# Kernel optimization log

Hardware: AMD Instinct MI355X
Metric: run time of the kernel (lower is better)

Reference implementation:

```python
import jax, jax.numpy as jnp
import numpy as np

B, SQ, SD, H = 64, 64, 512, 128


def setup_inputs() -> dict:
    key = jax.random.key(0)
    k1, k2, k3, k4, k5 = jax.random.split(key, 5)
    q = jax.random.normal(k1, (B, SQ, H), dtype=jnp.float32)
    d_pos = jax.random.normal(k2, (B, SD, H), dtype=jnp.float32)
    d_neg = jax.random.normal(k3, (B, SD, H), dtype=jnp.float32)
    mask_pos = jax.random.randint(k4, (B, SD), 0, 2, dtype=jnp.int32).at[:, 0].set(1)
    mask_neg = jax.random.randint(k5, (B, SD), 0, 2, dtype=jnp.int32).at[:, 0].set(1)
    return {"q": q, "d_pos": d_pos, "d_neg": d_neg,
            "mask_pos": mask_pos, "mask_neg": mask_neg}


def _colbert_maxsim(q, d, mask):
    # q: [a, s, h], d: [b, t, h], mask: [b, t] -> scores [a, b]
    simis = jnp.einsum('ash,bth->abst', q, d)            # [a, b, s, t]
    simis = jnp.where(mask[None, :, None, :] == 0, -jnp.inf, simis)
    return simis.max(axis=3).sum(axis=2)                 # max over t, sum over s


def reference(q, d_pos, d_neg, mask_pos, mask_neg):
    # Concatenate pos and in-batch-negative score blocks -> [B, 2B]
    distances = jnp.concatenate(
        [_colbert_maxsim(q, d_pos, mask_pos),
         _colbert_maxsim(q, d_neg, mask_neg)], axis=1)
    labels = jnp.arange(q.shape[0])
    logp = jax.nn.log_softmax(distances, axis=1)
    loss = -jnp.take_along_axis(logp, labels[:, None], axis=1).mean()
    return loss
```

## Files before the change

kernel.cpp:

```cpp
#include <hip/hip_runtime.h>
#include <hip/hip_bf16.h>
#include <math.h>
#include <stdint.h>

#define BB 64
#define SQN 64
#define SDN 512
#define HH 128

typedef __attribute__((ext_vector_type(8))) short bf16x8;
typedef __attribute__((ext_vector_type(16))) float f32x16;

__device__ __forceinline__ short f2bf(float f) {
  union { float f; unsigned u; } x; x.f = f;
  unsigned r = x.u + 0x7fffu + ((x.u >> 16) & 1u);
  return (short)(r >> 16);
}

__device__ __forceinline__ void gl_lds16(const short* g, short* l) {
  __builtin_amdgcn_global_load_lds(
      (const __attribute__((address_space(1))) unsigned int*)g,
      (__attribute__((address_space(3))) unsigned int*)l, 16, 0, 0);
}

__global__ __launch_bounds__(256)
void convert_all(const float* __restrict__ q, const float* __restrict__ dp,
                 const float* __restrict__ dn,
                 const int* __restrict__ mp, const int* __restrict__ mn,
                 short* __restrict__ oq, short* __restrict__ od,
                 int* __restrict__ nchunks, int* __restrict__ nvalid,
                 int* __restrict__ counter) {
  const int D_BLOCKS = (2 * BB * SDN) / 8;
  if (blockIdx.x < D_BLOCKS) {
    const int bs = blockIdx.x >> 6;
    const int j0 = (blockIdx.x & 63) * 8;
    const int side = bs >> 6, b = bs & 63;
    const int* mask = (side ? mn : mp) + b * SDN;

    __shared__ int s_perm[8];
    __shared__ int s_pad32;

    if (threadIdx.x < 64) {
      const int ln = threadIdx.x;
      int mreg[8];
      #pragma unroll
      for (int it = 0; it < 8; ++it) mreg[it] = mask[it * 64 + ln];
      int run = 0;
      #pragma unroll
      for (int it = 0; it < 8; ++it) {
        unsigned long long bal = __ballot(mreg[it] != 0);
        int pos = run + __popcll(bal & ((1ull << ln) - 1ull));
        if (mreg[it]) {
          unsigned rel = (unsigned)(pos - j0);
          if (rel < 8u) s_perm[rel] = it * 64 + ln;
        }
        run += (int)__popcll(bal);
      }
      if (ln < 8 && j0 + ln >= run) s_perm[ln] = -1;
      if (ln == 0) {
        s_pad32 = (run + 31) & ~31;
        if (j0 == 0) {
          nchunks[bs] = ((run + 127) & ~127) >> 7;
          nvalid[bs]  = run;
        }
      }
    }
    __syncthreads();

    const int j = j0 + (threadIdx.x >> 5);
    if (j >= s_pad32) return;
    const int l32 = threadIdx.x & 31;
    const int src_t = s_perm[threadIdx.x >> 5];
    const float* srcmat = side ? dn : dp;
    float4 v = make_float4(0.f, 0.f, 0.f, 0.f);
    if (src_t >= 0)
      v = ((const float4*)(srcmat + ((size_t)b * SDN + src_t) * HH))[l32];
    short4 o; o.x = f2bf(v.x); o.y = f2bf(v.y); o.z = f2bf(v.z); o.w = f2bf(v.w);
    *(short4*)&od[((size_t)bs * SDN + j) * HH + l32 * 4] = o;
  } else {
    if (blockIdx.x == D_BLOCKS && threadIdx.x == 0) *counter = 0;
    int i = (blockIdx.x - D_BLOCKS) * 256 + threadIdx.x;
    float4 v = ((const float4*)q)[i];
    short4 o; o.x = f2bf(v.x); o.y = f2bf(v.y); o.z = f2bf(v.z); o.w = f2bf(v.w);
    *(short4*)&oq[i * 4] = o;
  }
}

#define ITS_OF(bi_, tc_) \
  (((tc_) == nchv[bi_] - 1) ? (((nvv[bi_] - ((tc_) << 7) + 31) >> 5) << 1) : 8)

__global__ __launch_bounds__(256, 2)
void maxsim_kernel(const short* __restrict__ qb,
                   const short* __restrict__ dc,
                   const int* __restrict__ nchunks,
                   const int* __restrict__ nvalid,
                   float* __restrict__ scores,
                   int* __restrict__ counter,
                   float* __restrict__ out) {
  const int lid  = blockIdx.x + 16 * blockIdx.y;
  const int xcd  = lid & 7;
  const int slot = lid >> 3;
  const int aslc = slot & 15;
  const int bs0  = (xcd + 8 * (slot >> 4)) * 4;

  __shared__ __align__(16) short d_lds[2][128 * 128];

  const int tid = threadIdx.x;
  const int ln  = tid & 63;
  const int w   = tid >> 6;
  const int l31 = ln & 31;
  const int kh  = ln >> 5;
  const int a   = aslc * 4 + w;

  int nchv[4], nvv[4];
  #pragma unroll
  for (int i = 0; i < 4; ++i) {
    nchv[i] = nchunks[bs0 + i];
    nvv[i]  = nvalid[bs0 + i];
  }

  bf16x8 qfrag[2][8];
  #pragma unroll
  for (int half = 0; half < 2; ++half) {
    const short* qrow = qb + ((size_t)a * SQN + half * 32 + l31) * HH + kh * 8;
    #pragma unroll
    for (int kc = 0; kc < 8; ++kc)
      qfrag[half][kc] = *(const bf16x8*)(qrow + kc * 16);
  }

  float rmaxh[2] = {0.f, 0.f};

  int cur_its = ITS_OF(0, 0);

  {
    const short* dsrc = dc + (size_t)bs0 * SDN * HH;
    #pragma unroll
    for (int it = 0; it < 8; ++it) {
      if (it < cur_its) {
        int f = it * 256 + tid;
        int row = f >> 4;
        int c = (f & 15) ^ (row & 15);
        gl_lds16(&dsrc[row * HH + c * 8], &d_lds[0][(it * 256 + w * 64) * 8]);
      }
    }
  }
  __syncthreads();

  int bi = 0, tc = 0, buf = 0;
  for (;;) {
    int nbi = bi, ntc = tc + 1;
    if (ntc == nchv[bi]) { ntc = 0; nbi = bi + 1; }
    const bool hn = (nbi < 4);
    const int nxt_its = hn ? ITS_OF(nbi, ntc) : 0;

    if (hn) {
      const short* dsrc = dc + ((size_t)(bs0 + nbi) * SDN + ntc * 128) * HH;
      short* dst = &d_lds[buf ^ 1][0];
      #pragma unroll
      for (int it = 0; it < 8; ++it) {
        if (it < nxt_its) {
          int f = it * 256 + tid;
          int row = f >> 4;
          int c = (f & 15) ^ (row & 15);
          gl_lds16(&dsrc[row * HH + c * 8], &dst[(it * 256 + w * 64) * 8]);
        }
      }
    }

    const int ntt = cur_its >> 1;
    const short* bufp = &d_lds[buf][0];
    #pragma unroll
    for (int tt = 0; tt < 4; ++tt) {
      if (tt < ntt) {
        int trow = tt * 32 + l31;
        int tm = trow & 15;
        const short* bbase = &bufp[trow * HH];
        f32x16 acc0 = {0,0,0,0,0,0,0,0,0,0,0,0,0,0,0,0};
        f32x16 acc1 = {0,0,0,0,0,0,0,0,0,0,0,0,0,0,0,0};
        #pragma unroll
        for (int kc = 0; kc < 8; ++kc) {
          int c = (kc * 2 + kh) ^ tm;
          bf16x8 dfrag = *(const bf16x8*)&bbase[c * 8];
          acc0 = __builtin_amdgcn_mfma_f32_32x32x16_bf16(dfrag, qfrag[0][kc], acc0, 0, 0, 0);
          acc1 = __builtin_amdgcn_mfma_f32_32x32x16_bf16(dfrag, qfrag[1][kc], acc1, 0, 0, 0);
        }
        float m0 = acc0[0], m1 = acc1[0];
        #pragma unroll
        for (int r = 1; r < 16; ++r) {
          m0 = fmaxf(m0, acc0[r]);
          m1 = fmaxf(m1, acc1[r]);
        }
        rmaxh[0] = fmaxf(rmaxh[0], m0);
        rmaxh[1] = fmaxf(rmaxh[1], m1);
      }
    }

    if (ntc == 0) {
      float v0 = fmaxf(rmaxh[0], __shfl_xor(rmaxh[0], 32));
      float v1 = fmaxf(rmaxh[1], __shfl_xor(rmaxh[1], 32));
      float s = v0 + v1;
      s += __shfl_xor(s, 1);  s += __shfl_xor(s, 2);  s += __shfl_xor(s, 4);
      s += __shfl_xor(s, 8);  s += __shfl_xor(s, 16);
      if (ln == 0)
        __hip_atomic_store(&scores[(size_t)a * (2 * BB) + bs0 + bi], s,
                           __ATOMIC_RELAXED, __HIP_MEMORY_SCOPE_AGENT);
      rmaxh[0] = 0.f; rmaxh[1] = 0.f;
    }

    __syncthreads();
    if (!hn) break;
    bi = nbi; tc = ntc; buf ^= 1; cur_its = nxt_its;
  }

  asm volatile("s_waitcnt vmcnt(0)" ::: "memory");
  __shared__ int s_ticket;
  if (tid == 0)
    s_ticket = __hip_atomic_fetch_add(counter, 1,
                                      __ATOMIC_RELAXED, __HIP_MEMORY_SCOPE_AGENT);
  __syncthreads();
  if (s_ticket != 511) return;

  __shared__ float part[16];
  #pragma unroll
  for (int q8 = 0; q8 < 4; ++q8) {
    int vp = w * 4 + q8;
    float acc = 0.f;
    #pragma unroll
    for (int i = 0; i < 4; ++i) {
      int r = vp * 4 + i;
      float v0 = __hip_atomic_load(&scores[r * 128 + ln],
                                   __ATOMIC_RELAXED, __HIP_MEMORY_SCOPE_AGENT);
      float v1 = __hip_atomic_load(&scores[r * 128 + 64 + ln],
                                   __ATOMIC_RELAXED, __HIP_MEMORY_SCOPE_AGENT);
      float mx = fmaxf(v0, v1);
      #pragma unroll
      for (int off = 32; off >= 1; off >>= 1) mx = fmaxf(mx, __shfl_xor(mx, off));
      float e = __expf(v0 - mx) + __expf(v1 - mx);
      #pragma unroll
      for (int off = 32; off >= 1; off >>= 1) e += __shfl_xor(e, off);
      float lse = mx + __logf(e);
      float diag = __shfl(v0, r);
      acc += lse - diag;
    }
    if (ln == 0) part[vp] = acc;
  }
  __syncthreads();
  if (w == 0) {
    float v = (ln < 16) ? part[ln] : 0.f;
    #pragma unroll
    for (int off = 8; off >= 1; off >>= 1) v += __shfl_xor(v, off);
    if (ln == 0) out[0] = v * (1.0f / 64.0f);
  }
}

extern "C" void kernel_launch(void* const* d_in, const int* in_sizes, int n_in,
                              void* d_out, int out_size, void* d_ws, size_t ws_size,
                              hipStream_t stream) {
  const float* q        = (const float*)d_in[0];
  const float* d_pos    = (const float*)d_in[1];
  const float* d_neg    = (const float*)d_in[2];
  const int*   mask_pos = (const int*)d_in[3];
  const int*   mask_neg = (const int*)d_in[4];

  short* q_bf = (short*)d_ws;
  short* d_c  = q_bf + (size_t)BB * SQN * HH;
  int*   nchunks = (int*)(d_c + (size_t)2 * BB * SDN * HH);
  int*   nvalid  = nchunks + 128;
  float* scores  = (float*)(nvalid + 128);
  int*   counter = (int*)(scores + 64 * 128);

  const int D_BLOCKS = (2 * BB * SDN) / 8;
  const int Q_BLOCKS = (BB * SQN * HH / 4) / 256;
  convert_all<<<D_BLOCKS + Q_BLOCKS, 256, 0, stream>>>(
      q, d_pos, d_neg, mask_pos, mask_neg, q_bf, d_c, nchunks, nvalid, counter);

  dim3 grid(16 , 32 );
  maxsim_kernel<<<grid, 256, 0, stream>>>(q_bf, d_c, nchunks, nvalid, scores,
                                          counter, (float*)d_out);
}
```

Baseline: 126.8 us.

## Split doc chunk across waves, each wave reusing D tile for two queries

The maxsim kernel now gives each wave its own 32-row slice of every 128-row document chunk and its own double-buffered LDS ring. Each wave keeps fragments for two queries in registers, so every loaded D fragment feeds four MFMAs instead of two. The grid doubles to 1024 blocks, and waves combine their per-query row maxima through LDS with a barrier only at document boundaries, replacing the per-chunk __syncthreads. The trade-offs are more query registers per lane, full 32-row loads even when a partial chunk has fewer valid rows, and the nchunks array being recomputed from nvalid.

```diff
diff --git a/kernel.cpp b/kernel.cpp
--- a/kernel.cpp
+++ b/kernel.cpp
@@ -28,8 +28,7 @@
                  const float* __restrict__ dn,
                  const int* __restrict__ mp, const int* __restrict__ mn,
                  short* __restrict__ oq, short* __restrict__ od,
-                 int* __restrict__ nchunks, int* __restrict__ nvalid,
-                 int* __restrict__ counter) {
+                 int* __restrict__ nvalid, int* __restrict__ counter) {
   const int D_BLOCKS = (2 * BB * SDN) / 8;
   if (blockIdx.x < D_BLOCKS) {
     const int bs = blockIdx.x >> 6;
@@ -59,10 +58,7 @@
       if (ln < 8 && j0 + ln >= run) s_perm[ln] = -1;
       if (ln == 0) {
         s_pad32 = (run + 31) & ~31;
-        if (j0 == 0) {
-          nchunks[bs] = ((run + 127) & ~127) >> 7;
-          nvalid[bs]  = run;
-        }
+        if (j0 == 0) nvalid[bs] = run;
       }
     }
     __syncthreads();
@@ -86,163 +82,191 @@
   }
 }
 
-#define ITS_OF(bi_, tc_) \
-  (((tc_) == nchv[bi_] - 1) ? (((nvv[bi_] - ((tc_) << 7) + 31) >> 5) << 1) : 8)
-
 __global__ __launch_bounds__(256, 2)
 void maxsim_kernel(const short* __restrict__ qb,
                    const short* __restrict__ dc,
-                   const int* __restrict__ nchunks,
                    const int* __restrict__ nvalid,
                    float* __restrict__ scores,
                    int* __restrict__ counter,
                    float* __restrict__ out) {
-  const int lid  = blockIdx.x + 16 * blockIdx.y;
-  const int xcd  = lid & 7;
-  const int slot = lid >> 3;
-  const int aslc = slot & 15;
-  const int bs0  = (xcd + 8 * (slot >> 4)) * 4;
-
-  __shared__ __align__(16) short d_lds[2][128 * 128];
+  const int lid   = blockIdx.x + 32 * blockIdx.y;
+  const int xcd   = lid & 7;
+  const int slot  = lid >> 3;
+  const int aslot = slot & 31;
+  const int bs0   = (xcd + 8 * (slot >> 5)) * 4;
+
+  __shared__ __align__(16) short d_lds[4][2][32 * 128];
+  __shared__ float s_fin[4 * 2 * 2 * 32];
+  __shared__ int s_ticket;
+  __shared__ float part[16];
 
   const int tid = threadIdx.x;
   const int ln  = tid & 63;
   const int w   = tid >> 6;
   const int l31 = ln & 31;
   const int kh  = ln >> 5;
-  const int a   = aslc * 4 + w;
-
-  int nchv[4], nvv[4];
+
+  int nvv[4], nch[4];
   #pragma unroll
   for (int i = 0; i < 4; ++i) {
-    nchv[i] = nchunks[bs0 + i];
-    nvv[i]  = nvalid[bs0 + i];
-  }
-
-  bf16x8 qfrag[2][8];
+    nvv[i] = nvalid[bs0 + i];
+    nch[i] = (nvv[i] + 127) >> 7;
+  }
+
+  bf16x8 qf[2][2][8];
   #pragma unroll
-  for (int half = 0; half < 2; ++half) {
-    const short* qrow = qb + ((size_t)a * SQN + half * 32 + l31) * HH + kh * 8;
-    #pragma unroll
-    for (int kc = 0; kc < 8; ++kc)
-      qfrag[half][kc] = *(const bf16x8*)(qrow + kc * 16);
-  }
-
-  float rmaxh[2] = {0.f, 0.f};
-
-  int cur_its = ITS_OF(0, 0);
-
+  for (int qi = 0; qi < 2; ++qi) {
+    #pragma unroll
+    for (int half = 0; half < 2; ++half) {
+      const short* qrow = qb + ((size_t)(aslot * 2 + qi) * SQN + half * 32 + l31) * HH + kh * 8;
+      #pragma unroll
+      for (int kc = 0; kc < 8; ++kc)
+        qf[qi][half][kc] = *(const bf16x8*)(qrow + kc * 16);
+    }
+  }
+
+  int src_off[8];
   {
-    const short* dsrc = dc + (size_t)bs0 * SDN * HH;
+    int r0 = ln >> 4, c0 = ln & 15;
     #pragma unroll
     for (int it = 0; it < 8; ++it) {
-      if (it < cur_its) {
-        int f = it * 256 + tid;
-        int row = f >> 4;
-        int c = (f & 15) ^ (row & 15);
-        gl_lds16(&dsrc[row * HH + c * 8], &d_lds[0][(it * 256 + w * 64) * 8]);
-      }
-    }
-  }
+      int row_rel = it * 4 + r0;
+      src_off[it] = row_rel * HH + (c0 ^ (row_rel & 15)) * 8;
+    }
+  }
+  int rd_off[8];
+  #pragma unroll
+  for (int kc = 0; kc < 8; ++kc)
+    rd_off[kc] = l31 * HH + (((kc * 2 + kh) ^ (l31 & 15)) * 8);
+
+  float rmax[2][2] = {{0.f, 0.f}, {0.f, 0.f}};
+
+  auto STAGE = [&](int pbi, int ptc, int rs) {
+    const short* dsrc = dc + (((size_t)(bs0 + pbi) * SDN) + ptc * 128 + w * 32) * HH;
+    short* slotp = &d_lds[w][rs][0];
+    #pragma unroll
+    for (int it = 0; it < 8; ++it)
+      gl_lds16(dsrc + src_off[it], slotp + it * 512);
+  };
+
+  int pbi = 0, ptc = 0;
+  STAGE(pbi, ptc, 0);
+  if (++ptc == nch[pbi]) { ptc = 0; ++pbi; }
+
+  int cbi = 0, ctc = 0, ring = 0;
+  for (;;) {
+    const bool hn = (pbi < 4);
+    if (hn) {
+      STAGE(pbi, ptc, ring ^ 1);
+      if (++ptc == nch[pbi]) { ptc = 0; ++pbi; }
+      asm volatile("s_waitcnt vmcnt(8)" ::: "memory");
+    } else {
+      asm volatile("s_waitcnt vmcnt(0)" ::: "memory");
+    }
+
+    const int rows = nvv[cbi] - (ctc << 7);
+    if (w * 32 < rows) {
+      const short* slotp = &d_lds[w][ring][0];
+      bf16x8 dv[8];
+      #pragma unroll
+      for (int kc = 0; kc < 8; ++kc)
+        dv[kc] = *(const bf16x8*)(slotp + rd_off[kc]);
+      f32x16 a00 = {0,0,0,0,0,0,0,0,0,0,0,0,0,0,0,0};
+      f32x16 a01 = {0,0,0,0,0,0,0,0,0,0,0,0,0,0,0,0};
+      f32x16 a10 = {0,0,0,0,0,0,0,0,0,0,0,0,0,0,0,0};
+      f32x16 a11 = {0,0,0,0,0,0,0,0,0,0,0,0,0,0,0,0};
+      #pragma unroll
+      for (int kc = 0; kc < 8; ++kc) {
+        a00 = __builtin_amdgcn_mfma_f32_32x32x16_bf16(dv[kc], qf[0][0][kc], a00, 0, 0, 0);
+        a01 = __builtin_amdgcn_mfma_f32_32x32x16_bf16(dv[kc], qf[0][1][kc], a01, 0, 0, 0);
+        a10 = __builtin_amdgcn_mfma_f32_32x32x16_bf16(dv[kc], qf[1][0][kc], a10, 0, 0, 0);
+        a11 = __builtin_amdgcn_mfma_f32_32x32x16_bf16(dv[kc], qf[1][1][kc], a11, 0, 0, 0);
+      }
+      float m00 = a00[0], m01 = a01[0], m10 = a10[0], m11 = a11[0];
+      #pragma unroll
+      for (int r = 1; r < 16; ++r) {
+        m00 = fmaxf(m00, a00[r]);  m01 = fmaxf(m01, a01[r]);
+        m10 = fmaxf(m10, a10[r]);  m11 = fmaxf(m11, a11[r]);
+      }
+      rmax[0][0] = fmaxf(rmax[0][0], m00);
+      rmax[0][1] = fmaxf(rmax[0][1], m01);
+      rmax[1][0] = fmaxf(rmax[1][0], m10);
+      rmax[1][1] = fmaxf(rmax[1][1], m11);
+    }
+
+    const int obi = cbi;
+    if (++ctc == nch[cbi]) {
+      ctc = 0; ++cbi;
+      float v[2][2];
+      #pragma unroll
+      for (int qi = 0; qi < 2; ++qi)
+        #pragma unroll
+        for (int half = 0; half < 2; ++half)
+          v[qi][half] = fmaxf(rmax[qi][half], __shfl_xor(rmax[qi][half], 32));
+      if (kh == 0) {
+        #pragma unroll
+        for (int qi = 0; qi < 2; ++qi)
+          #pragma unroll
+          for (int half = 0; half < 2; ++half)
+            s_fin[((w * 2 + qi) * 2 + half) * 32 + l31] = v[qi][half];
+      }
+      asm volatile("s_waitcnt lgkmcnt(0)" ::: "memory");
+      __builtin_amdgcn_s_barrier();
+      if (w < 2) {
+        float m0 = s_fin[((0 * 2 + w) * 2 + 0) * 32 + l31];
+        float m1 = s_fin[((0 * 2 + w) * 2 + 1) * 32 + l31];
+        #pragma unroll
+        for (int ww = 1; ww < 4; ++ww) {
+          m0 = fmaxf(m0, s_fin[((ww * 2 + w) * 2 + 0) * 32 + l31]);
+          m1 = fmaxf(m1, s_fin[((ww * 2 + w) * 2 + 1) * 32 + l31]);
+        }
+        float s = m0 + m1;
+        s += __shfl_xor(s, 1);  s += __shfl_xor(s, 2);  s += __shfl_xor(s, 4);
+        s += __shfl_xor(s, 8);  s += __shfl_xor(s, 16);
+        if (ln == 0)
+          __hip_atomic_store(&scores[(size_t)(aslot * 2 + w) * (2 * BB) + bs0 + obi],
+                             s, __ATOMIC_RELAXED, __HIP_MEMORY_SCOPE_AGENT);
+      }
+      __builtin_amdgcn_s_barrier();
+      rmax[0][0] = 0.f; rmax[0][1] = 0.f; rmax[1][0] = 0.f; rmax[1][1] = 0.f;
+    }
+
+    if (cbi == 4) break;
+    ring ^= 1;
+  }
+
+  asm volatile("s_waitcnt vmcnt(0)" ::: "memory");
   __syncthreads();
-
-  int bi = 0, tc = 0, buf = 0;
-  for (;;) {
-    int nbi = bi, ntc = tc + 1;
-    if (ntc == nchv[bi]) { ntc = 0; nbi = bi + 1; }
-    const bool hn = (nbi < 4);
-    const int nxt_its = hn ? ITS_OF(nbi, ntc) : 0;
-
-    if (hn) {
-      const short* dsrc = dc + ((size_t)(bs0 + nbi) * SDN + ntc * 128) * HH;
-      short* dst = &d_lds[buf ^ 1][0];
-      #pragma unroll
-      for (int it = 0; it < 8; ++it) {
-        if (it < nxt_its) {
-          int f = it * 256 + tid;
-          int row = f >> 4;
-          int c = (f & 15) ^ (row & 15);
-          gl_lds16(&dsrc[row * HH + c * 8], &dst[(it * 256 + w * 64) * 8]);
-        }
-      }
-    }
-
-    const int ntt = cur_its >> 1;
-    const short* bufp = &d_lds[buf][0];
-    #pragma unroll
-    for (int tt = 0; tt < 4; ++tt) {
-      if (tt < ntt) {
-        int trow = tt * 32 + l31;
-        int tm = trow & 15;
-        const short* bbase = &bufp[trow * HH];
-        f32x16 acc0 = {0,0,0,0,0,0,0,0,0,0,0,0,0,0,0,0};
-        f32x16 acc1 = {0,0,0,0,0,0,0,0,0,0,0,0,0,0,0,0};
-        #pragma unroll
-        for (int kc = 0; kc < 8; ++kc) {
-          int c = (kc * 2 + kh) ^ tm;
-          bf16x8 dfrag = *(const bf16x8*)&bbase[c * 8];
-          acc0 = __builtin_amdgcn_mfma_f32_32x32x16_bf16(dfrag, qfrag[0][kc], acc0, 0, 0, 0);
-          acc1 = __builtin_amdgcn_mfma_f32_32x32x16_bf16(dfrag, qfrag[1][kc], acc1, 0, 0, 0);
-        }
-        float m0 = acc0[0], m1 = acc1[0];
-        #pragma unroll
-        for (int r = 1; r < 16; ++r) {
-          m0 = fmaxf(m0, acc0[r]);
-          m1 = fmaxf(m1, acc1[r]);
-        }
-        rmaxh[0] = fmaxf(rmaxh[0], m0);
-        rmaxh[1] = fmaxf(rmaxh[1], m1);
-      }
-    }
-
-    if (ntc == 0) {
-      float v0 = fmaxf(rmaxh[0], __shfl_xor(rmaxh[0], 32));
-      float v1 = fmaxf(rmaxh[1], __shfl_xor(rmaxh[1], 32));
-      float s = v0 + v1;
-      s += __shfl_xor(s, 1);  s += __shfl_xor(s, 2);  s += __shfl_xor(s, 4);
-      s += __shfl_xor(s, 8);  s += __shfl_xor(s, 16);
-      if (ln == 0)
-        __hip_atomic_store(&scores[(size_t)a * (2 * BB) + bs0 + bi], s,
-                           __ATOMIC_RELAXED, __HIP_MEMORY_SCOPE_AGENT);
-      rmaxh[0] = 0.f; rmaxh[1] = 0.f;
-    }
-
-    __syncthreads();
-    if (!hn) break;
-    bi = nbi; tc = ntc; buf ^= 1; cur_its = nxt_its;
-  }
-
-  asm volatile("s_waitcnt vmcnt(0)" ::: "memory");
-  __shared__ int s_ticket;
   if (tid == 0)
     s_ticket = __hip_atomic_fetch_add(counter, 1,
                                       __ATOMIC_RELAXED, __HIP_MEMORY_SCOPE_AGENT);
   __syncthreads();
-  if (s_ticket != 511) return;
-
-  __shared__ float part[16];
-  #pragma unroll
-  for (int q8 = 0; q8 < 4; ++q8) {
-    int vp = w * 4 + q8;
-    float acc = 0.f;
-    #pragma unroll
-    for (int i = 0; i < 4; ++i) {
-      int r = vp * 4 + i;
-      float v0 = __hip_atomic_load(&scores[r * 128 + ln],
-                                   __ATOMIC_RELAXED, __HIP_MEMORY_SCOPE_AGENT);
-      float v1 = __hip_atomic_load(&scores[r * 128 + 64 + ln],
-                                   __ATOMIC_RELAXED, __HIP_MEMORY_SCOPE_AGENT);
-      float mx = fmaxf(v0, v1);
-      #pragma unroll
-      for (int off = 32; off >= 1; off >>= 1) mx = fmaxf(mx, __shfl_xor(mx, off));
-      float e = __expf(v0 - mx) + __expf(v1 - mx);
-      #pragma unroll
-      for (int off = 32; off >= 1; off >>= 1) e += __shfl_xor(e, off);
-      float lse = mx + __logf(e);
-      float diag = __shfl(v0, r);
-      acc += lse - diag;
-    }
-    if (ln == 0) part[vp] = acc;
+  if (s_ticket != 1023) return;
+
+  {
+    #pragma unroll
+    for (int q8 = 0; q8 < 4; ++q8) {
+      int vp = w * 4 + q8;
+      float acc = 0.f;
+      #pragma unroll
+      for (int i = 0; i < 4; ++i) {
+        int r = vp * 4 + i;
+        float v0 = __hip_atomic_load(&scores[r * 128 + ln],
+                                     __ATOMIC_RELAXED, __HIP_MEMORY_SCOPE_AGENT);
+        float v1 = __hip_atomic_load(&scores[r * 128 + 64 + ln],
+                                     __ATOMIC_RELAXED, __HIP_MEMORY_SCOPE_AGENT);
+        float mx = fmaxf(v0, v1);
+        #pragma unroll
+        for (int off = 32; off >= 1; off >>= 1) mx = fmaxf(mx, __shfl_xor(mx, off));
+        float e = __expf(v0 - mx) + __expf(v1 - mx);
+        #pragma unroll
+        for (int off = 32; off >= 1; off >>= 1) e += __shfl_xor(e, off);
+        float lse = mx + __logf(e);
+        float diag = __shfl(v0, r);
+        acc += lse - diag;
+      }
+      if (ln == 0) part[vp] = acc;
+    }
   }
   __syncthreads();
   if (w == 0) {
@@ -264,17 +288,16 @@
 
   short* q_bf = (short*)d_ws;
   short* d_c  = q_bf + (size_t)BB * SQN * HH;
-  int*   nchunks = (int*)(d_c + (size_t)2 * BB * SDN * HH);
-  int*   nvalid  = nchunks + 128;
+  int*   nvalid  = (int*)(d_c + (size_t)2 * BB * SDN * HH);
   float* scores  = (float*)(nvalid + 128);
   int*   counter = (int*)(scores + 64 * 128);
 
   const int D_BLOCKS = (2 * BB * SDN) / 8;
   const int Q_BLOCKS = (BB * SQN * HH / 4) / 256;
   convert_all<<<D_BLOCKS + Q_BLOCKS, 256, 0, stream>>>(
-      q, d_pos, d_neg, mask_pos, mask_neg, q_bf, d_c, nchunks, nvalid, counter);
-
-  dim3 grid(16 , 32 );
-  maxsim_kernel<<<grid, 256, 0, stream>>>(q_bf, d_c, nchunks, nvalid, scores,
+      q, d_pos, d_neg, mask_pos, mask_neg, q_bf, d_c, nvalid, counter);
+
+  dim3 grid(32, 32);
+  maxsim_kernel<<<grid, 256, 0, stream>>>(q_bf, d_c, nvalid, scores,
                                           counter, (float*)d_out);
 }
```

Result: slower. 141.5 us (+11.7%).
